# Kernel optimization log

Measured on AMD Instinct MI355X. Metric: run time of the kernel, lower is better.

The kernel has to match this reference:

```python
import jax, jax.numpy as jnp
import numpy as np

N = 20000      # nodes per set
E = 320000     # edges per graph (avg degree 16)
C = 256        # embed_channels
H = 4          # num_heads
D = C // H     # head dim
P = 3          # pos_dim


def setup_inputs() -> dict:
    key = jax.random.key(0)
    ks = jax.random.split(key, 16)
    f32 = jnp.float32
    rn = lambda k, s, sc=1.0: jax.random.normal(k, s, dtype=f32) * sc
    ri = lambda k: jax.random.randint(k, (2, E), 0, N, dtype=jnp.int32)
    return {
        "feat1": rn(ks[0], (N, C)),
        "coord1": rn(ks[1], (N, P)),
        "feat2": rn(ks[2], (N, C)),
        "coord2": rn(ks[3], (N, P)),
        "Wqkv1": rn(ks[4], (C, 6 * C), 0.02),
        "bqkv1": jnp.zeros((6 * C,), f32),
        "Wqkv2": rn(ks[5], (C, 6 * C), 0.02),
        "bqkv2": jnp.zeros((6 * C,), f32),
        "Wproj1": rn(ks[6], (2 * C, C), 0.02),
        "bproj1": jnp.zeros((C,), f32),
        "Wproj2": rn(ks[7], (2 * C, C), 0.02),
        "bproj2": jnp.zeros((C,), f32),
        "Wrpe": rn(ks[8], (P, C), 0.02),
        "brpe": jnp.zeros((C,), f32),
        "graph1": ri(ks[9]),
        "graph2": ri(ks[10]),
        "graph12": ri(ks[11]),
        "graph21": ri(ks[12]),
    }


def _edge_attention(key_, query, value, g, n, rpe=None):
    # key_/query/value: [n_src_or_dst, H, D]; g: [2, E]; rpe: [E, H, D] or None
    k = key_[g[1]]          # [E, H, D] gather source
    q = query[g[0]]         # [E, H, D] gather destination
    v = value[g[1]]         # [E, H, D]
    s = k * q
    if rpe is not None:
        s = s + rpe
    s = s.sum(-1)           # [E, H] per-edge, per-head score
    dst = g[0]
    m = jax.ops.segment_max(s, dst, num_segments=n)      # [n, H]
    e = jnp.exp(s - m[dst])
    z = jax.ops.segment_sum(e, dst, num_segments=n)      # [n, H]
    a = e / z[dst]                                       # scatter-softmax
    out = jax.ops.segment_sum(a[..., None] * v, dst, num_segments=n)  # [n, H, D]
    return out.reshape(n, H * D)


def _qkv(feat, W, b):
    n = feat.shape[0]
    qkv = (feat @ W + b).reshape(n, 6, H, D)
    return tuple(qkv[:, i] for i in range(6))  # q_a,k_a,v_a,q_b,k_b,v_b


def reference(feat1, coord1, feat2, coord2, Wqkv1, bqkv1, Wqkv2, bqkv2,
              Wproj1, bproj1, Wproj2, bproj2, Wrpe, brpe,
              graph1, graph2, graph12, graph21):
    n1, n2 = feat1.shape[0], feat2.shape[0]
    q11, k11, v11, q12, k12, v12 = _qkv(feat1, Wqkv1, bqkv1)
    q21, k21, v21, q22, k22, v22 = _qkv(feat2, Wqkv2, bqkv2)

    rpe1 = ((coord1[graph1[0]] - coord1[graph1[1]]) @ Wrpe + brpe).reshape(-1, H, D)
    rpe2 = ((coord2[graph2[0]] - coord2[graph2[1]]) @ Wrpe + brpe).reshape(-1, H, D)

    feat11 = _edge_attention(k11, q11, v11, graph1, n1, rpe1)
    feat22 = _edge_attention(k22, q22, v22, graph2, n2, rpe2)
    feat12 = _edge_attention(k21, q12, v21, graph21, n1)
    feat21 = _edge_attention(k12, q21, v12, graph12, n2)

    out1 = jnp.concatenate([feat11, feat12], axis=1) @ Wproj1 + bproj1
    out2 = jnp.concatenate([feat22, feat21], axis=1) @ Wproj2 + bproj2
    return (out1, out2)
```

## Files before the change

### kernel.cpp

```cpp
#include <hip/hip_runtime.h>
#include <stdint.h>
#include <stddef.h>

#define N_NODES 20000
#define N_EDGES 320000
#define NCH 79

typedef unsigned short u16;
typedef __attribute__((ext_vector_type(8))) short bf16x8;
typedef __attribute__((ext_vector_type(8))) unsigned short u16x8;
typedef __attribute__((ext_vector_type(4))) float f32x4;

__device__ __forceinline__ float bf2f(u16 u) {
    union { unsigned int i; float f; } v; v.i = ((unsigned int)u) << 16; return v.f;
}
__device__ __forceinline__ u16 f2bf(float f) {
    union { float f; unsigned int i; } v; v.f = f;
    unsigned int x = v.i;
    unsigned int r = x + 0x7fffu + ((x >> 16) & 1u);
    return (u16)(r >> 16);
}
__device__ __forceinline__ int clampi(int v, int lo, int hi) {
    return v < lo ? lo : (v > hi ? hi : v);
}
__device__ __forceinline__ float ld1(const void* p, size_t i, int f32) {
    return f32 ? ((const float*)p)[i] : bf2f(((const u16*)p)[i]);
}

__device__ __forceinline__ void async_ld16(void* lds, const void* g) {
    __builtin_amdgcn_global_load_lds(
        (const __attribute__((address_space(1))) unsigned int*)g,
        (__attribute__((address_space(3))) unsigned int*)lds,
        16, 0, 0);
}

__device__ __forceinline__ int xcd_chunk(int b, int nwg) {
    int x = b & 7, idx = b >> 3;
    int q = nwg >> 3, r = nwg & 7;
    return ((x < r) ? (x * (q + 1)) : (r * (q + 1) + (x - r) * q)) + idx;
}

__global__ void marker_kernel(u16* out, u16 code) { out[threadIdx.x] = code; }

__global__ void detect_kernel(const void* feat, int* diag) {
    int lane = threadIdx.x;
    int weird = 0;
    const u16* p = (const u16*)feat;
    for (int i = lane; i < 512; i += 64) {
        float v = bf2f(p[i]);
        float a = fabsf(v);
        if (!(a <= 1e4f) || (a != 0.f && a < 1e-6f)) weird++;
    }
#pragma unroll
    for (int off = 32; off > 0; off >>= 1) weird += __shfl_xor(weird, off, 64);
    if (lane == 0) { diag[0] = 123456; diag[1] = (weird > 51) ? 1 : 0; diag[2] = 0; }
}

__global__ void rpe_sums_kernel(const void* __restrict__ Wrpe, const void* __restrict__ brpe,
                                float* __restrict__ out, const int* __restrict__ dflag) {
    int f32 = dflag[0];
    int t = threadIdx.x;
    if (t < 12) {
        int p = t >> 2, h = t & 3;
        float s = 0.f;
        for (int d = 0; d < 64; ++d) s += ld1(Wrpe, p * 256 + h * 64 + d, f32);
        out[t] = s;
    } else if (t < 16) {
        int h = t - 12;
        float s = 0.f;
        for (int d = 0; d < 64; ++d) s += ld1(brpe, h * 64 + d, f32);
        out[12 + h] = s;
    }
}

__global__ __launch_bounds__(256) void coordproj_kernel(const void* __restrict__ coord,
                                                        const int* __restrict__ dflag,
                                                        const float* __restrict__ rs,
                                                        float* __restrict__ proj, int n) {
    int i = blockIdx.x * 256 + threadIdx.x;
    if (i >= n * 4) return;
    int f32 = dflag[0];
    int node = i >> 2, h = i & 3;
    float s = ld1(coord, (size_t)node * 3 + 0, f32) * rs[0 * 4 + h]
            + ld1(coord, (size_t)node * 3 + 1, f32) * rs[1 * 4 + h]
            + ld1(coord, (size_t)node * 3 + 2, f32) * rs[2 * 4 + h];
    proj[i] = s;
}

__global__ __launch_bounds__(256) void transpose_w_kernel(const void* __restrict__ W,
                                                          const int* __restrict__ dflag,
                                                          u16* __restrict__ Wt, int K, int N) {
    int f32 = dflag[0];
    int i = blockIdx.x * 256 + threadIdx.x;
    if (i >= K * N) return;
    int n = i / K, k = i - n * K;
    Wt[i] = f2bf(ld1(W, (size_t)k * N + n, f32));
}

__global__ __launch_bounds__(256) void tobf16_kernel(
        const void* __restrict__ a, const void* __restrict__ b,
        const int* __restrict__ dflag, u16* __restrict__ oa, u16* __restrict__ ob) {
    const int PER = N_NODES * 256 / 8;
    int idx = blockIdx.x * 256 + threadIdx.x;
    if (idx >= 2 * PER) return;
    int set = idx >= PER;
    int j = (idx - set * PER) * 8;
    const void* src = set ? b : a;
    u16* dst = set ? ob : oa;
    int f32 = dflag[0];
    u16x8 o;
    if (f32) {
        const float* p = (const float*)src + j;
        float4 u0 = *(const float4*)p, u1 = *(const float4*)(p + 4);
        o[0] = f2bf(u0.x); o[1] = f2bf(u0.y); o[2] = f2bf(u0.z); o[3] = f2bf(u0.w);
        o[4] = f2bf(u1.x); o[5] = f2bf(u1.y); o[6] = f2bf(u1.z); o[7] = f2bf(u1.w);
    } else {
        o = *(const u16x8*)((const u16*)src + j);
    }
    *(u16x8*)(dst + j) = o;
}

__global__ __launch_bounds__(256) void count_kernel(
        const int* __restrict__ g0, const int* __restrict__ g1,
        const int* __restrict__ g2, const int* __restrict__ g3,
        int* __restrict__ deg, u16* __restrict__ rank) {
    int b = blockIdx.x;
    int gi = b & 3;
    int h = (b >> 2) & 1;
    int e = (b >> 2) * 256 + (int)threadIdx.x;
    if (e >= N_EDGES) return;
    const int* g = (gi == 0) ? g0 : (gi == 1) ? g1 : (gi == 2) ? g2 : g3;
    int dst = clampi(g[e], 0, N_NODES - 1);
    int pos = atomicAdd(&deg[(gi * 2 + h) * N_NODES + dst], 1);
    pos = pos & 0x7fff;
    rank[(size_t)gi * N_EDGES + e] = (u16)((h << 15) | pos);
}

__global__ __launch_bounds__(256) void scan1_kernel(const int* __restrict__ cur,
                                                    int* __restrict__ tmp,
                                                    int* __restrict__ csum) {
    int b = blockIdx.x;
    int g = b / NCH, ch = b - g * NCH;
    int tid = threadIdx.x;
    int i = ch * 256 + tid;
    const int* d0 = cur + (g * 2 + 0) * N_NODES;
    const int* d1 = cur + (g * 2 + 1) * N_NODES;
    int val = (i < N_NODES) ? (d0[i] + d1[i]) : 0;
    __shared__ int buf[256];
    buf[tid] = val;
    __syncthreads();
    for (int off = 1; off < 256; off <<= 1) {
        int x = (tid >= off) ? buf[tid - off] : 0;
        __syncthreads();
        buf[tid] += x;
        __syncthreads();
    }
    if (i < N_NODES) tmp[g * N_NODES + i] = buf[tid] - val;
    if (tid == 255) csum[g * NCH + ch] = buf[255];
}

__global__ __launch_bounds__(256) void scan2_kernel(const int* __restrict__ csum,
                                                    int* __restrict__ coff,
                                                    int* __restrict__ rowptr) {
    int g = blockIdx.x;
    int tid = threadIdx.x;
    int v = (tid < NCH) ? csum[g * NCH + tid] : 0;
    __shared__ int buf[256];
    buf[tid] = v;
    __syncthreads();
    for (int off = 1; off < 256; off <<= 1) {
        int x = (tid >= off) ? buf[tid - off] : 0;
        __syncthreads();
        buf[tid] += x;
        __syncthreads();
    }
    if (tid < NCH) coff[g * NCH + tid] = buf[tid] - v;
    if (tid == 255) rowptr[g * (N_NODES + 1) + N_NODES] = buf[255];
}

__global__ __launch_bounds__(256) void scan3_kernel(const int* __restrict__ tmp,
                                                    const int* __restrict__ coff,
                                                    int* __restrict__ rowptr) {
    int b = blockIdx.x;
    int g = b / NCH, ch = b - g * NCH;
    int i = ch * 256 + (int)threadIdx.x;
    if (i < N_NODES)
        rowptr[g * (N_NODES + 1) + i] = tmp[g * N_NODES + i] + coff[g * NCH + ch];
}

__global__ __launch_bounds__(256) void fill_kernel(
        const int* __restrict__ g0, const int* __restrict__ g1,
        const int* __restrict__ g2, const int* __restrict__ g3,
        const int* __restrict__ rowptr, const int* __restrict__ cur,
        const u16* __restrict__ rank, u16* __restrict__ col) {
    int b = blockIdx.x;
    int gi = b & 3;
    int e = (b >> 2) * 256 + (int)threadIdx.x;
    if (e >= N_EDGES) return;
    const int* g = (gi == 0) ? g0 : (gi == 1) ? g1 : (gi == 2) ? g2 : g3;
    int dst = clampi(g[e], 0, N_NODES - 1);
    int src = clampi(g[N_EDGES + e], 0, N_NODES - 1);
    u16 rk = rank[(size_t)gi * N_EDGES + e];
    int h = rk >> 15, r = rk & 0x7fff;
    int base = h ? cur[(gi * 2 + 0) * N_NODES + dst] : 0;
    int pos = rowptr[gi * (N_NODES + 1) + dst] + base + r;
    if (pos >= 0 && pos < N_EDGES)
        col[(size_t)gi * N_EDGES + pos] = (u16)src;
}

__global__ __launch_bounds__(256) void gemm_mfma(
        const void* __restrict__ A, int lda, const int* __restrict__ aflag,
        const u16* __restrict__ Bt,
        const void* __restrict__ bias, size_t biasoff, const int* __restrict__ bflag,
        void* __restrict__ C, size_t coff, int ldc, const int* __restrict__ cflag,
        int M, int N, int K) {
    __shared__ __align__(16) u16 As[128 * 40];
    __shared__ __align__(16) u16 Bs[128 * 40];
    const int f32a = aflag[0], f32b = bflag[0], f32c = cflag[0];
    const int t = threadIdx.x;
    const int lane = t & 63, wv = t >> 6;
    const int wm = (wv >> 1) * 64, wn = (wv & 1) * 64;
    const int m0 = blockIdx.y * 128, n0 = blockIdx.x * 128;
    const int l15 = lane & 15, lq = lane >> 4;

    f32x4 acc[4][4];
#pragma unroll
    for (int i = 0; i < 4; ++i)
#pragma unroll
        for (int j = 0; j < 4; ++j) acc[i][j] = (f32x4){0.f, 0.f, 0.f, 0.f};

    const int sr = t >> 1, skc = (t & 1) * 16;

    for (int k0 = 0; k0 < K; k0 += 32) {
        __syncthreads();
        {
            __align__(16) u16 tmp[16];
            int gm = m0 + sr;
            if (gm < M) {
                if (f32a) {
                    const float* ap = (const float*)A + (size_t)gm * lda + k0 + skc;
#pragma unroll
                    for (int i = 0; i < 16; i += 4) {
                        float4 u = *(const float4*)(ap + i);
                        tmp[i] = f2bf(u.x); tmp[i + 1] = f2bf(u.y);
                        tmp[i + 2] = f2bf(u.z); tmp[i + 3] = f2bf(u.w);
                    }
                } else {
                    const u16* ap = (const u16*)A + (size_t)gm * lda + k0 + skc;
                    *(u16x8*)&tmp[0] = *(const u16x8*)ap;
                    *(u16x8*)&tmp[8] = *(const u16x8*)(ap + 8);
                }
            } else {
#pragma unroll
                for (int i = 0; i < 16; ++i) tmp[i] = 0;
            }
            *(u16x8*)&As[sr * 40 + skc] = *(u16x8*)&tmp[0];
            *(u16x8*)&As[sr * 40 + skc + 8] = *(u16x8*)&tmp[8];
        }
        {
            const u16* bp = Bt + (size_t)(n0 + sr) * K + k0 + skc;
            u16x8 b0 = *(const u16x8*)bp;
            u16x8 b1 = *(const u16x8*)(bp + 8);
            *(u16x8*)&Bs[sr * 40 + skc] = b0;
            *(u16x8*)&Bs[sr * 40 + skc + 8] = b1;
        }
        __syncthreads();
        bf16x8 af[4], bfr[4];
#pragma unroll
        for (int mt = 0; mt < 4; ++mt)
            af[mt] = *(const bf16x8*)&As[(wm + mt * 16 + l15) * 40 + lq * 8];
#pragma unroll
        for (int nt = 0; nt < 4; ++nt)
            bfr[nt] = *(const bf16x8*)&Bs[(wn + nt * 16 + l15) * 40 + lq * 8];
#pragma unroll
        for (int mt = 0; mt < 4; ++mt)
#pragma unroll
            for (int nt = 0; nt < 4; ++nt)
                acc[mt][nt] = __builtin_amdgcn_mfma_f32_16x16x32_bf16(af[mt], bfr[nt], acc[mt][nt], 0, 0, 0);
    }
#pragma unroll
    for (int mt = 0; mt < 4; ++mt) {
#pragma unroll
        for (int nt = 0; nt < 4; ++nt) {
            int gn = n0 + wn + nt * 16 + l15;
            float bb = ld1(bias, biasoff + gn, f32b);
#pragma unroll
            for (int r = 0; r < 4; ++r) {
                int gm = m0 + wm + mt * 16 + lq * 4 + r;
                if (gm < M) {
                    float v = acc[mt][nt][r] + bb;
                    size_t ic = coff + (size_t)gm * ldc + gn;
                    if (f32c) ((float*)C)[ic] = v;
                    else      ((u16*)C)[ic] = f2bf(v);
                }
            }
        }
    }
}

__global__ __launch_bounds__(256, 4) void gemm_pipe(
        const u16* __restrict__ A1, const u16* __restrict__ A2, int K,
        const u16* __restrict__ Bt1, const u16* __restrict__ Bt2,
        const void* __restrict__ bias1, const void* __restrict__ bias2,
        const int* __restrict__ bflag,
        void* __restrict__ C, size_t coff1, size_t coff2, int ldc,
        const int* __restrict__ cflag,
        int M, int nr, int nc) {
    __shared__ __align__(16) u16 S[16384];
    u16* As = S;
    u16* Bs = S + 8192;
    const int f32b = bflag[0], f32c = cflag[0];
    const int t = threadIdx.x;
    const int half = nr * nc;
    const int nwg = 2 * half;
    int b = xcd_chunk(blockIdx.x, nwg);
    const int set = (b >= half) ? 1 : 0;
    b -= set * half;
    const int c = b % nc, r = b / nc;
    const int m0 = r * 128, n0 = c * 128;
    const u16* A   = set ? A2 : A1;
    const u16* Bt  = set ? Bt2 : Bt1;
    const void* bias = set ? bias2 : bias1;
    const size_t coff = set ? coff2 : coff1;

    const int lane = t & 63, wv = t >> 6;
    const int wm = (wv >> 1) * 64, wn = (wv & 1) * 64;
    const int l15 = lane & 15, lq = lane >> 4;

    const int srow8 = lane >> 3;
    const int sgsw  = ((lane & 7) ^ srow8) * 8;
    const u16* agp[4];
    const u16* bgp[4];
    u16 *lap[4], *lbp[4];
#pragma unroll
    for (int i = 0; i < 4; ++i) {
        int ra = m0 + wv * 32 + i * 8 + srow8; if (ra > M - 1) ra = M - 1;
        int rb = n0 + wv * 32 + i * 8 + srow8;
        agp[i] = A  + (size_t)ra * K + sgsw;
        bgp[i] = Bt + (size_t)rb * K + sgsw;
        lap[i] = &As[(wv * 32 + i * 8) * 64];
        lbp[i] = &Bs[(wv * 32 + i * 8) * 64];
    }
    const int l7 = l15 & 7;

    f32x4 acc[4][4];
#pragma unroll
    for (int i = 0; i < 4; ++i)
#pragma unroll
        for (int j = 0; j < 4; ++j) acc[i][j] = (f32x4){0.f, 0.f, 0.f, 0.f};

    for (int k0 = 0; k0 < K; k0 += 64) {
        __syncthreads();
#pragma unroll
        for (int i = 0; i < 4; ++i) async_ld16(lap[i], agp[i] + k0);
#pragma unroll
        for (int i = 0; i < 4; ++i) async_ld16(lbp[i], bgp[i] + k0);
        __syncthreads();
#pragma unroll
        for (int h2 = 0; h2 < 2; ++h2) {
            const int gq = lq + h2 * 4;
            bf16x8 af[4], bfr[4];
#pragma unroll
            for (int mt = 0; mt < 4; ++mt)
                af[mt] = *(const bf16x8*)&As[(wm + mt * 16 + l15) * 64 + ((gq ^ l7) << 3)];
#pragma unroll
            for (int nt = 0; nt < 4; ++nt)
                bfr[nt] = *(const bf16x8*)&Bs[(wn + nt * 16 + l15) * 64 + ((gq ^ l7) << 3)];
#pragma unroll
            for (int mt = 0; mt < 4; ++mt)
#pragma unroll
                for (int nt = 0; nt < 4; ++nt)
                    acc[mt][nt] = __builtin_amdgcn_mfma_f32_16x16x32_bf16(
                        bfr[nt], af[mt], acc[mt][nt], 0, 0, 0);
        }
    }

    if (!f32c) {
        u16* Cs = S;
#pragma unroll
        for (int p = 0; p < 2; ++p) {
            __syncthreads();
            if ((wv >> 1) == p) {
#pragma unroll
                for (int nt = 0; nt < 4; ++nt) {
                    int lc = wn + nt * 16 + lq * 4;
                    int gn0 = n0 + lc;
                    float b0 = ld1(bias, gn0 + 0, f32b);
                    float b1 = ld1(bias, gn0 + 1, f32b);
                    float b2 = ld1(bias, gn0 + 2, f32b);
                    float b3 = ld1(bias, gn0 + 3, f32b);
#pragma unroll
                    for (int mt = 0; mt < 4; ++mt) {
                        ushort4 o;
                        o.x = f2bf(acc[mt][nt][0] + b0);
                        o.y = f2bf(acc[mt][nt][1] + b1);
                        o.z = f2bf(acc[mt][nt][2] + b2);
                        o.w = f2bf(acc[mt][nt][3] + b3);
                        *(ushort4*)&Cs[(mt * 16 + l15) * 128 + (lc ^ (l15 << 3))] = o;
                    }
                }
            }
            __syncthreads();
#pragma unroll
            for (int it = 0; it < 4; ++it) {
                int idx = it * 256 + t;
                int row = idx >> 4, ch = idx & 15;
                int gm = m0 + p * 64 + row;
                if (gm < M)
                    *(u16x8*)((u16*)C + coff + (size_t)gm * ldc + n0 + ch * 8) =
                        *(const u16x8*)&Cs[row * 128 + ((ch * 8) ^ ((row & 15) << 3))];
            }
        }
    } else {
        float* Cs = (float*)S;
#pragma unroll
        for (int p = 0; p < 4; ++p) {
            __syncthreads();
            if ((wv >> 1) == (p >> 1)) {
                int mtb = (p & 1) * 2;
#pragma unroll
                for (int nt = 0; nt < 4; ++nt) {
                    int lc = wn + nt * 16 + lq * 4;
                    int gn0 = n0 + lc;
                    float b0 = ld1(bias, gn0 + 0, f32b);
                    float b1 = ld1(bias, gn0 + 1, f32b);
                    float b2 = ld1(bias, gn0 + 2, f32b);
                    float b3 = ld1(bias, gn0 + 3, f32b);
#pragma unroll
                    for (int mi = 0; mi < 2; ++mi) {
                        int mt = mtb + mi;
                        f32x4 o;
                        o[0] = acc[mt][nt][0] + b0;
                        o[1] = acc[mt][nt][1] + b1;
                        o[2] = acc[mt][nt][2] + b2;
                        o[3] = acc[mt][nt][3] + b3;
                        *(f32x4*)&Cs[(mi * 16 + l15) * 128 + lc] = o;
                    }
                }
            }
            __syncthreads();
#pragma unroll
            for (int it = 0; it < 4; ++it) {
                int idx = it * 256 + t;
                int row = idx >> 5, ch = idx & 31;
                int gm = m0 + p * 32 + row;
                if (gm < M)
                    *(float4*)((float*)C + coff + (size_t)gm * ldc + n0 + ch * 4) =
                        *(const float4*)&Cs[row * 128 + ch * 4];
            }
        }
    }
}

__global__ __launch_bounds__(256) void attn3_kernel(
        const u16* __restrict__ Q, const u16* __restrict__ Kp, const u16* __restrict__ Vp,
        const int* __restrict__ rowptr, const u16* __restrict__ col,
        const float* __restrict__ projN, const float* __restrict__ projS,
        const float* __restrict__ rb, int use_rpe,
        u16* __restrict__ outp, int ldt) {
    int lane = threadIdx.x & 63;
    int node = blockIdx.x * 4 + (threadIdx.x >> 6);
    if (node >= N_NODES) return;
    int h = lane >> 4;
    int off = h * 64 + (lane & 15) * 4;

    ushort4 qu = *(const ushort4*)(Q + (size_t)node * ldt + off);
    float q0 = bf2f(qu.x), q1 = bf2f(qu.y), q2 = bf2f(qu.z), q3 = bf2f(qu.w);
    float base = use_rpe ? (projN[node * 4 + h] + rb[h]) : 0.f;

    float m = -1e30f, l = 0.f, a0 = 0.f, a1 = 0.f, a2 = 0.f, a3 = 0.f;
    int e0 = rowptr[node], e1 = rowptr[node + 1];
    e0 = clampi(e0, 0, N_EDGES);
    e1 = clampi(e1, e0, N_EDGES);
    int e = e0;
    for (; e + 4 <= e1; e += 4) {
        int s0 = clampi((int)col[e + 0], 0, N_NODES - 1);
        int s1 = clampi((int)col[e + 1], 0, N_NODES - 1);
        int s2 = clampi((int)col[e + 2], 0, N_NODES - 1);
        int s3 = clampi((int)col[e + 3], 0, N_NODES - 1);
        ushort4 k0 = *(const ushort4*)(Kp + (size_t)s0 * ldt + off);
        ushort4 k1 = *(const ushort4*)(Kp + (size_t)s1 * ldt + off);
        ushort4 k2 = *(const ushort4*)(Kp + (size_t)s2 * ldt + off);
        ushort4 k3 = *(const ushort4*)(Kp + (size_t)s3 * ldt + off);
        ushort4 v0 = *(const ushort4*)(Vp + (size_t)s0 * ldt + off);
        ushort4 v1 = *(const ushort4*)(Vp + (size_t)s1 * ldt + off);
        ushort4 v2 = *(const ushort4*)(Vp + (size_t)s2 * ldt + off);
        ushort4 v3 = *(const ushort4*)(Vp + (size_t)s3 * ldt + off);
        float t0 = q0 * bf2f(k0.x) + q1 * bf2f(k0.y) + q2 * bf2f(k0.z) + q3 * bf2f(k0.w);
        float t1 = q0 * bf2f(k1.x) + q1 * bf2f(k1.y) + q2 * bf2f(k1.z) + q3 * bf2f(k1.w);
        float t2 = q0 * bf2f(k2.x) + q1 * bf2f(k2.y) + q2 * bf2f(k2.z) + q3 * bf2f(k2.w);
        float t3 = q0 * bf2f(k3.x) + q1 * bf2f(k3.y) + q2 * bf2f(k3.z) + q3 * bf2f(k3.w);
#pragma unroll
        for (int sh = 1; sh <= 8; sh <<= 1) {
            t0 += __shfl_xor(t0, sh, 64);
            t1 += __shfl_xor(t1, sh, 64);
            t2 += __shfl_xor(t2, sh, 64);
            t3 += __shfl_xor(t3, sh, 64);
        }
        if (use_rpe) {
            t0 += base - projS[s0 * 4 + h];
            t1 += base - projS[s1 * 4 + h];
            t2 += base - projS[s2 * 4 + h];
            t3 += base - projS[s3 * 4 + h];
        }
        float mx = fmaxf(fmaxf(fmaxf(t0, t1), fmaxf(t2, t3)), m);
        float sc = __expf(m - mx);
        float p0 = __expf(t0 - mx), p1 = __expf(t1 - mx);
        float p2 = __expf(t2 - mx), p3 = __expf(t3 - mx);
        l = l * sc + (p0 + p1 + p2 + p3);
        a0 = a0 * sc + p0 * bf2f(v0.x) + p1 * bf2f(v1.x) + p2 * bf2f(v2.x) + p3 * bf2f(v3.x);
        a1 = a1 * sc + p0 * bf2f(v0.y) + p1 * bf2f(v1.y) + p2 * bf2f(v2.y) + p3 * bf2f(v3.y);
        a2 = a2 * sc + p0 * bf2f(v0.z) + p1 * bf2f(v1.z) + p2 * bf2f(v2.z) + p3 * bf2f(v3.z);
        a3 = a3 * sc + p0 * bf2f(v0.w) + p1 * bf2f(v1.w) + p2 * bf2f(v2.w) + p3 * bf2f(v3.w);
        m = mx;
    }
    for (; e < e1; ++e) {
        int src = clampi((int)col[e], 0, N_NODES - 1);
        ushort4 ku = *(const ushort4*)(Kp + (size_t)src * ldt + off);
        ushort4 vu = *(const ushort4*)(Vp + (size_t)src * ldt + off);
        float tv = q0 * bf2f(ku.x) + q1 * bf2f(ku.y) + q2 * bf2f(ku.z) + q3 * bf2f(ku.w);
        tv += __shfl_xor(tv, 1, 64);
        tv += __shfl_xor(tv, 2, 64);
        tv += __shfl_xor(tv, 4, 64);
        tv += __shfl_xor(tv, 8, 64);
        if (use_rpe) tv += base - projS[src * 4 + h];
        float mn = fmaxf(m, tv);
        float sc = __expf(m - mn), p = __expf(tv - mn);
        l = l * sc + p;
        a0 = a0 * sc + p * bf2f(vu.x);
        a1 = a1 * sc + p * bf2f(vu.y);
        a2 = a2 * sc + p * bf2f(vu.z);
        a3 = a3 * sc + p * bf2f(vu.w);
        m = mn;
    }
    float inv = l > 0.f ? 1.f / l : 0.f;
    ushort4 o;
    o.x = f2bf(a0 * inv); o.y = f2bf(a1 * inv); o.z = f2bf(a2 * inv); o.w = f2bf(a3 * inv);
    *(ushort4*)(outp + (size_t)node * 512 + off) = o;
}

extern "C" void kernel_launch(void* const* d_in, const int* in_sizes, int n_in,
                              void* d_out, int out_size, void* d_ws, size_t ws_size,
                              hipStream_t stream) {
    const void* feat1  = d_in[0];
    const void* coord1 = d_in[1];
    const void* feat2  = d_in[2];
    const void* coord2 = d_in[3];
    const void* Wqkv1  = d_in[4];
    const void* bqkv1  = d_in[5];
    const void* Wqkv2  = d_in[6];
    const void* bqkv2  = d_in[7];
    const void* Wproj1 = d_in[8];
    const void* bproj1 = d_in[9];
    const void* Wproj2 = d_in[10];
    const void* bproj2 = d_in[11];
    const void* Wrpe   = d_in[12];
    const void* brpe   = d_in[13];
    const int* graph1  = (const int*)d_in[14];
    const int* graph2  = (const int*)d_in[15];
    const int* graph12 = (const int*)d_in[16];
    const int* graph21 = (const int*)d_in[17];
    u16* out = (u16*)d_out;

    {
        static const int expect[18] = {
            N_NODES * 256, N_NODES * 3, N_NODES * 256, N_NODES * 3,
            256 * 1536, 1536, 256 * 1536, 1536,
            512 * 256, 256, 512 * 256, 256,
            3 * 256, 256,
            2 * N_EDGES, 2 * N_EDGES, 2 * N_EDGES, 2 * N_EDGES };
        bool ok = (n_in == 18) && (out_size == 2 * N_NODES * 256);
        if (ok) for (int i = 0; i < 18; ++i) if (in_sizes[i] != expect[i]) ok = false;
        if (!ok) { marker_kernel<<<1, 16, 0, stream>>>(out, 0x4496 ); return; }
    }

    char* w = (char*)d_ws;
    size_t off = 0;
    auto alloc = [&](size_t bytes) { void* p = w + off; off += (bytes + 255) & ~(size_t)255; return p; };
    int* rowptr  = (int*)alloc(4ull * (N_NODES + 1) * 4);
    int* cur     = (int*)alloc(8ull * N_NODES * 4);
    u16* col     = (u16*)alloc(4ull * N_EDGES * 2);
    u16* rank    = (u16*)alloc(4ull * N_EDGES * 2);
    int* tmpscan = (int*)alloc(4ull * N_NODES * 4);
    int* csum    = (int*)alloc(4ull * NCH * 4);
    int* coffb   = (int*)alloc(4ull * NCH * 4);
    float* rpe_s = (float*)alloc(64);
    int* diag    = (int*)alloc(256);
    float* proj1 = (float*)alloc((size_t)N_NODES * 4 * 4);
    float* proj2 = (float*)alloc((size_t)N_NODES * 4 * 4);
    u16* Wqkv1t  = (u16*)alloc((size_t)1536 * 256 * 2);
    u16* Wqkv2t  = (u16*)alloc((size_t)1536 * 256 * 2);
    u16* Wproj1t = (u16*)alloc((size_t)256 * 512 * 2);
    u16* Wproj2t = (u16*)alloc((size_t)256 * 512 * 2);
    size_t off_common = off;

    u16* cat = (u16*)alloc(2ull * N_NODES * 512 * 2);
    u16* T1  = (u16*)alloc(2ull * N_NODES * 1536 * 2);
    u16* T2  = T1 + (size_t)N_NODES * 1536;
    bool big = (off <= ws_size);
    u16* Told = nullptr;
    if (!big) {
        off = off_common;
        cat  = (u16*)alloc((size_t)N_NODES * 512 * 2);
        Told = (u16*)alloc((size_t)N_NODES * 768 * 2);
        if (off > ws_size) {
            marker_kernel<<<1, 16, 0, stream>>>(out, 0x447A );
            return;
        }
    }
    const int* dF = diag + 1;
    const int* dZ = diag + 2;

    const int NP1 = N_NODES + 1;
    hipMemsetAsync(cur, 0, 8ull * N_NODES * 4, stream);
    hipMemsetAsync(diag, 0, 256, stream);

    detect_kernel<<<1, 64, 0, stream>>>(feat1, diag);
    rpe_sums_kernel<<<1, 64, 0, stream>>>(Wrpe, brpe, rpe_s, dF);
    coordproj_kernel<<<(N_NODES * 4 + 255) / 256, 256, 0, stream>>>(coord1, dF, rpe_s, proj1, N_NODES);
    coordproj_kernel<<<(N_NODES * 4 + 255) / 256, 256, 0, stream>>>(coord2, dF, rpe_s, proj2, N_NODES);
    transpose_w_kernel<<<(1536 * 256 + 255) / 256, 256, 0, stream>>>(Wqkv1, dF, Wqkv1t, 256, 1536);
    transpose_w_kernel<<<(1536 * 256 + 255) / 256, 256, 0, stream>>>(Wqkv2, dF, Wqkv2t, 256, 1536);
    transpose_w_kernel<<<(256 * 512 + 255) / 256, 256, 0, stream>>>(Wproj1, dF, Wproj1t, 512, 256);
    transpose_w_kernel<<<(256 * 512 + 255) / 256, 256, 0, stream>>>(Wproj2, dF, Wproj2t, 512, 256);

    const int EB = 4 * N_EDGES / 256;
    count_kernel<<<EB, 256, 0, stream>>>(graph1, graph2, graph12, graph21, cur, rank);
    scan1_kernel<<<4 * NCH, 256, 0, stream>>>(cur, tmpscan, csum);
    scan2_kernel<<<4, 256, 0, stream>>>(csum, coffb, rowptr);
    scan3_kernel<<<4 * NCH, 256, 0, stream>>>(tmpscan, coffb, rowptr);
    fill_kernel<<<EB, 256, 0, stream>>>(graph1, graph2, graph12, graph21, rowptr, cur, rank, col);

    const dim3 blk(256);
    const int AG = (N_NODES + 3) / 4;

    if (big) {
        u16* cat1 = cat;
        u16* cat2 = cat + (size_t)N_NODES * 512;
        u16* featb1 = cat;
        u16* featb2 = cat + (size_t)N_NODES * 256;
        const int NROW = (N_NODES + 127) / 128;

        tobf16_kernel<<<(2 * N_NODES * 256 / 8 + 255) / 256, blk, 0, stream>>>(
            feat1, feat2, dF, featb1, featb2);

        gemm_pipe<<<dim3(2 * NROW * 12), blk, 0, stream>>>(
            featb1, featb2, 256, Wqkv1t, Wqkv2t, bqkv1, bqkv2, dF,
            T1, 0, (size_t)N_NODES * 1536, 1536, dZ, N_NODES, NROW, 12);

        attn3_kernel<<<AG, blk, 0, stream>>>(T1 + 0, T1 + 256, T1 + 512,
                                             rowptr + 0 * NP1, col + 0 * (size_t)N_EDGES,
                                             proj1, proj1, rpe_s + 12, 1, cat1 + 0, 1536);
        attn3_kernel<<<AG, blk, 0, stream>>>(T1 + 768, T2 + 256, T2 + 512,
                                             rowptr + 3 * NP1, col + 3 * (size_t)N_EDGES,
                                             nullptr, nullptr, rpe_s + 12, 0, cat1 + 256, 1536);
        attn3_kernel<<<AG, blk, 0, stream>>>(T2 + 768, T2 + 1024, T2 + 1280,
                                             rowptr + 1 * NP1, col + 1 * (size_t)N_EDGES,
                                             proj2, proj2, rpe_s + 12, 1, cat2 + 0, 1536);
        attn3_kernel<<<AG, blk, 0, stream>>>(T2 + 0, T1 + 1024, T1 + 1280,
                                             rowptr + 2 * NP1, col + 2 * (size_t)N_EDGES,
                                             nullptr, nullptr, rpe_s + 12, 0, cat2 + 256, 1536);

        gemm_pipe<<<dim3(2 * NROW * 2), blk, 0, stream>>>(
            cat1, cat2, 512, Wproj1t, Wproj2t, bproj1, bproj2, dF,
            out, 0, (size_t)N_NODES * 256, 256, dF, N_NODES, NROW, 2);
        return;
    }

    u16* T = Told;
    const int GY = (N_NODES + 127) / 128;
    gemm_mfma<<<dim3(6, GY), blk, 0, stream>>>(feat1, 256, dF, Wqkv1t + 0 * 256,
                                               bqkv1, 0, dF, T, 0, 768, dZ, N_NODES, 768, 256);
    attn3_kernel<<<AG, blk, 0, stream>>>(T, T + 256, T + 512, rowptr + 0 * NP1, col + 0 * (size_t)N_EDGES,
                                         proj1, proj1, rpe_s + 12, 1, cat + 0, 768);
    gemm_mfma<<<dim3(2, GY), blk, 0, stream>>>(feat1, 256, dF, Wqkv1t + (size_t)768 * 256,
                                               bqkv1, 768, dF, T, 0, 768, dZ, N_NODES, 256, 256);
    gemm_mfma<<<dim3(4, GY), blk, 0, stream>>>(feat2, 256, dF, Wqkv2t + (size_t)256 * 256,
                                               bqkv2, 256, dF, T, 256, 768, dZ, N_NODES, 512, 256);
    attn3_kernel<<<AG, blk, 0, stream>>>(T, T + 256, T + 512, rowptr + 3 * NP1, col + 3 * (size_t)N_EDGES,
                                         nullptr, nullptr, rpe_s + 12, 0, cat + 256, 768);
    gemm_mfma<<<dim3(2, GY), blk, 0, stream>>>(cat, 512, dZ, Wproj1t,
                                               bproj1, 0, dF, out, 0, 256, dF, N_NODES, 256, 512);

    gemm_mfma<<<dim3(6, GY), blk, 0, stream>>>(feat2, 256, dF, Wqkv2t + (size_t)768 * 256,
                                               bqkv2, 768, dF, T, 0, 768, dZ, N_NODES, 768, 256);
    attn3_kernel<<<AG, blk, 0, stream>>>(T, T + 256, T + 512, rowptr + 1 * NP1, col + 1 * (size_t)N_EDGES,
                                         proj2, proj2, rpe_s + 12, 1, cat + 0, 768);
    gemm_mfma<<<dim3(2, GY), blk, 0, stream>>>(feat2, 256, dF, Wqkv2t + 0,
                                               bqkv2, 0, dF, T, 0, 768, dZ, N_NODES, 256, 256);
    gemm_mfma<<<dim3(4, GY), blk, 0, stream>>>(feat1, 256, dF, Wqkv1t + (size_t)1024 * 256,
                                               bqkv1, 1024, dF, T, 256, 768, dZ, N_NODES, 512, 256);
    attn3_kernel<<<AG, blk, 0, stream>>>(T, T + 256, T + 512, rowptr + 2 * NP1, col + 2 * (size_t)N_EDGES,
                                         nullptr, nullptr, rpe_s + 12, 0, cat + 256, 768);
    gemm_mfma<<<dim3(2, GY), blk, 0, stream>>>(cat, 512, dZ, Wproj2t,
                                               bproj2, 0, dF, out, (size_t)N_NODES * 256, 256, dF,
                                               N_NODES, 256, 512);
}
```

Before: 506.3 us.

## Build CSR via per-block node-range shared-memory histograms instead of global atomics

```diff
diff --git a/kernel.cpp b/kernel.cpp
--- a/kernel.cpp
+++ b/kernel.cpp
@@ -5,6 +5,8 @@
 #define N_NODES 20000
 #define N_EDGES 320000
 #define NCH 79
+#define NB  64
+#define NPB 313
 
 typedef unsigned short u16;
 typedef __attribute__((ext_vector_type(8))) short bf16x8;
@@ -120,20 +122,33 @@
     *(u16x8*)(dst + j) = o;
 }
 
-__global__ __launch_bounds__(256) void count_kernel(
+__global__ __launch_bounds__(256) void count2_kernel(
         const int* __restrict__ g0, const int* __restrict__ g1,
         const int* __restrict__ g2, const int* __restrict__ g3,
-        int* __restrict__ deg, u16* __restrict__ rank) {
+        int* __restrict__ deg) {
     int b = blockIdx.x;
-    int gi = b & 3;
-    int h = (b >> 2) & 1;
-    int e = (b >> 2) * 256 + (int)threadIdx.x;
-    if (e >= N_EDGES) return;
+    int gi = b / NB, rb = b - gi * NB;
+    int lo = rb * NPB;
+    int hi = lo + NPB; if (hi > N_NODES) hi = N_NODES;
     const int* g = (gi == 0) ? g0 : (gi == 1) ? g1 : (gi == 2) ? g2 : g3;
-    int dst = clampi(g[e], 0, N_NODES - 1);
-    int pos = atomicAdd(&deg[(gi * 2 + h) * N_NODES + dst], 1);
-    pos = pos & 0x7fff;
-    rank[(size_t)gi * N_EDGES + e] = (u16)((h << 15) | pos);
+    __shared__ int hist[NPB];
+    for (int i = threadIdx.x; i < NPB; i += 256) hist[i] = 0;
+    __syncthreads();
+    for (int base = 0; base < N_EDGES; base += 1024) {
+        int idx = base + (int)threadIdx.x * 4;
+        if (idx + 3 < N_EDGES) {
+            int4 d4 = *(const int4*)&g[idx];
+#pragma unroll
+            for (int j = 0; j < 4; ++j) {
+                int dst = clampi(j == 0 ? d4.x : j == 1 ? d4.y : j == 2 ? d4.z : d4.w,
+                                 0, N_NODES - 1);
+                if (dst >= lo && dst < hi) atomicAdd(&hist[dst - lo], 1);
+            }
+        }
+    }
+    __syncthreads();
+    for (int i = threadIdx.x; i < NPB && lo + i < N_NODES; i += 256)
+        deg[gi * N_NODES + lo + i] = hist[i];
 }
 
 __global__ __launch_bounds__(256) void scan1_kernel(const int* __restrict__ cur,
@@ -143,9 +158,8 @@
     int g = b / NCH, ch = b - g * NCH;
     int tid = threadIdx.x;
     int i = ch * 256 + tid;
-    const int* d0 = cur + (g * 2 + 0) * N_NODES;
-    const int* d1 = cur + (g * 2 + 1) * N_NODES;
-    int val = (i < N_NODES) ? (d0[i] + d1[i]) : 0;
+    const int* d0 = cur + g * N_NODES;
+    int val = (i < N_NODES) ? d0[i] : 0;
     __shared__ int buf[256];
     buf[tid] = val;
     __syncthreads();
@@ -188,24 +202,37 @@
         rowptr[g * (N_NODES + 1) + i] = tmp[g * N_NODES + i] + coff[g * NCH + ch];
 }
 
-__global__ __launch_bounds__(256) void fill_kernel(
+__global__ __launch_bounds__(256) void fill2_kernel(
         const int* __restrict__ g0, const int* __restrict__ g1,
         const int* __restrict__ g2, const int* __restrict__ g3,
-        const int* __restrict__ rowptr, const int* __restrict__ cur,
-        const u16* __restrict__ rank, u16* __restrict__ col) {
+        const int* __restrict__ rowptr, u16* __restrict__ col) {
     int b = blockIdx.x;
-    int gi = b & 3;
-    int e = (b >> 2) * 256 + (int)threadIdx.x;
-    if (e >= N_EDGES) return;
+    int gi = b / NB, rb = b - gi * NB;
+    int lo = rb * NPB;
+    int hi = lo + NPB; if (hi > N_NODES) hi = N_NODES;
     const int* g = (gi == 0) ? g0 : (gi == 1) ? g1 : (gi == 2) ? g2 : g3;
-    int dst = clampi(g[e], 0, N_NODES - 1);
-    int src = clampi(g[N_EDGES + e], 0, N_NODES - 1);
-    u16 rk = rank[(size_t)gi * N_EDGES + e];
-    int h = rk >> 15, r = rk & 0x7fff;
-    int base = h ? cur[(gi * 2 + 0) * N_NODES + dst] : 0;
-    int pos = rowptr[gi * (N_NODES + 1) + dst] + base + r;
-    if (pos >= 0 && pos < N_EDGES)
-        col[(size_t)gi * N_EDGES + pos] = (u16)src;
+    const int* rp = rowptr + gi * (N_NODES + 1);
+    u16* cg = col + (size_t)gi * N_EDGES;
+    __shared__ int cnt[NPB];
+    for (int i = threadIdx.x; i < NPB; i += 256) cnt[i] = 0;
+    __syncthreads();
+    for (int base = 0; base < N_EDGES; base += 1024) {
+        int idx = base + (int)threadIdx.x * 4;
+        if (idx + 3 < N_EDGES) {
+            int4 d4 = *(const int4*)&g[idx];
+#pragma unroll
+            for (int j = 0; j < 4; ++j) {
+                int dst = clampi(j == 0 ? d4.x : j == 1 ? d4.y : j == 2 ? d4.z : d4.w,
+                                 0, N_NODES - 1);
+                if (dst >= lo && dst < hi) {
+                    int src = clampi(g[N_EDGES + idx + j], 0, N_NODES - 1);
+                    int r = atomicAdd(&cnt[dst - lo], 1);
+                    int pos = rp[dst] + r;
+                    if (pos >= 0 && pos < N_EDGES) cg[pos] = (u16)src;
+                }
+            }
+        }
+    }
 }
 
 __global__ __launch_bounds__(256) void gemm_mfma(
@@ -578,9 +605,8 @@
     size_t off = 0;
     auto alloc = [&](size_t bytes) { void* p = w + off; off += (bytes + 255) & ~(size_t)255; return p; };
     int* rowptr  = (int*)alloc(4ull * (N_NODES + 1) * 4);
-    int* cur     = (int*)alloc(8ull * N_NODES * 4);
+    int* cur     = (int*)alloc(4ull * N_NODES * 4);
     u16* col     = (u16*)alloc(4ull * N_EDGES * 2);
-    u16* rank    = (u16*)alloc(4ull * N_EDGES * 2);
     int* tmpscan = (int*)alloc(4ull * N_NODES * 4);
     int* csum    = (int*)alloc(4ull * NCH * 4);
     int* coffb   = (int*)alloc(4ull * NCH * 4);
@@ -612,7 +638,6 @@
     const int* dZ = diag + 2;
 
     const int NP1 = N_NODES + 1;
-    hipMemsetAsync(cur, 0, 8ull * N_NODES * 4, stream);
     hipMemsetAsync(diag, 0, 256, stream);
 
     detect_kernel<<<1, 64, 0, stream>>>(feat1, diag);
@@ -624,12 +649,11 @@
     transpose_w_kernel<<<(256 * 512 + 255) / 256, 256, 0, stream>>>(Wproj1, dF, Wproj1t, 512, 256);
     transpose_w_kernel<<<(256 * 512 + 255) / 256, 256, 0, stream>>>(Wproj2, dF, Wproj2t, 512, 256);
 
-    const int EB = 4 * N_EDGES / 256;
-    count_kernel<<<EB, 256, 0, stream>>>(graph1, graph2, graph12, graph21, cur, rank);
+    count2_kernel<<<4 * NB, 256, 0, stream>>>(graph1, graph2, graph12, graph21, cur);
     scan1_kernel<<<4 * NCH, 256, 0, stream>>>(cur, tmpscan, csum);
     scan2_kernel<<<4, 256, 0, stream>>>(csum, coffb, rowptr);
     scan3_kernel<<<4 * NCH, 256, 0, stream>>>(tmpscan, coffb, rowptr);
-    fill_kernel<<<EB, 256, 0, stream>>>(graph1, graph2, graph12, graph21, rowptr, cur, rank, col);
+    fill2_kernel<<<4 * NB, 256, 0, stream>>>(graph1, graph2, graph12, graph21, rowptr, col);
 
     const dim3 blk(256);
     const int AG = (N_NODES + 3) / 4;
```

Measured after the change: 952.1 us. 88.1% more time.
